# Kernel optimization log

Hardware: AMD Instinct MI355X
Metric: run time of the kernel (lower is better)

## Reference

```python
import jax, jax.numpy as jnp
import numpy as np

V, BLK, L, H, E = 50257, 1024, 12, 12, 768
HS = E // H
B = 2


def _ln(x, w, b, eps=1e-5):
    mu = jnp.mean(x, axis=-1, keepdims=True)
    var = jnp.mean((x - mu) ** 2, axis=-1, keepdims=True)
    return (x - mu) * jax.lax.rsqrt(var + eps) * w + b


def setup_inputs() -> dict:
    key = jax.random.key(0)
    ks = jax.random.split(key, 16)
    s = 0.02
    inp = {
        "x": jax.random.randint(ks[0], (B, BLK), 0, V),
        "tok_emb": jax.random.normal(ks[1], (V, E), jnp.float32) * s,
        "pos_emb": jax.random.normal(ks[2], (BLK, E), jnp.float32) * s,
        "qW": jax.random.normal(ks[3], (L, H, HS, E), jnp.float32) * s,
        "kW": jax.random.normal(ks[4], (L, H, HS, E), jnp.float32) * s,
        "vW": jax.random.normal(ks[5], (L, H, HS, E), jnp.float32) * s,
        "ln1_w": jnp.ones((L, E), jnp.float32),
        "ln1_b": jnp.zeros((L, E), jnp.float32),
        "fc1_w": jax.random.normal(ks[6], (L, 4 * E, E), jnp.float32) * s,
        "fc1_b": jnp.zeros((L, 4 * E), jnp.float32),
        "fc2_w": jax.random.normal(ks[7], (L, E, 4 * E), jnp.float32) * s,
        "fc2_b": jnp.zeros((L, E), jnp.float32),
        "ln2_w": jnp.ones((L, E), jnp.float32),
        "ln2_b": jnp.zeros((L, E), jnp.float32),
        "lnf_w": jnp.ones((E,), jnp.float32),
        "lnf_b": jnp.zeros((E,), jnp.float32),
        "lm_w": jax.random.normal(ks[8], (V, E), jnp.float32) * s,
    }
    return inp


def _gpt(x, tok_emb, pos_emb, qW, kW, vW, ln1_w, ln1_b, fc1_w, fc1_b,
         fc2_w, fc2_b, ln2_w, ln2_b, lnf_w, lnf_b, lm_w):
    T = x.shape[1]
    h = tok_emb[x] + pos_emb[None, :T]  # [B,T,E]
    scale = 1.0 / jnp.sqrt(jnp.asarray(E, h.dtype))  # C**0.5 with C=n_embd
    causal = jnp.tril(jnp.ones((T, T), bool))  # mask where tril==0
    for l in range(L):
        q = jnp.einsum("bte,hde->bthd", h, qW[l])
        k = jnp.einsum("bte,hde->bthd", h, kW[l])
        v = jnp.einsum("bte,hde->bthd", h, vW[l])
        # faithful to source: w = k @ q^T / sqrt(n_embd); rows index k, cols index q
        w = jnp.einsum("bshd,bthd->bhst", k, q) * scale
        w = jnp.where(causal[None, None], w, -jnp.inf)
        w = jax.nn.softmax(w, axis=-1)
        a = jnp.einsum("bhst,bthd->bshd", w, v)  # [B,T,H,HS]
        a = a.reshape(a.shape[0], T, E)  # head-major concat
        h = _ln(h + a, ln1_w[l], ln1_b[l])
        m = jax.nn.gelu(jnp.einsum("bte,fe->btf", h, fc1_w[l]) + fc1_b[l],
                        approximate=False)
        m = jnp.einsum("btf,ef->bte", m, fc2_w[l]) + fc2_b[l]
        h = _ln(h + m, ln2_w[l], ln2_b[l])
    h = _ln(h, lnf_w, lnf_b)
    return jnp.einsum("bte,ve->btv", h, lm_w)


def reference(x, tok_emb, pos_emb, qW, kW, vW, ln1_w, ln1_b, fc1_w, fc1_b,
              fc2_w, fc2_b, ln2_w, ln2_b, lnf_w, lnf_b, lm_w):
    return _gpt(x, tok_emb, pos_emb, qW, kW, vW, ln1_w, ln1_b, fc1_w, fc1_b,
                fc2_w, fc2_b, ln2_w, ln2_b, lnf_w, lnf_b, lm_w)
```

## Files before the change

kernel.cpp:

```cpp
#include <hip/hip_runtime.h>
#include <math.h>

typedef unsigned short u16;
typedef __attribute__((ext_vector_type(8))) short short8;
typedef __attribute__((ext_vector_type(8))) u16 ushort8_t;
typedef __attribute__((ext_vector_type(4))) u16 ushort4_t;
typedef __attribute__((ext_vector_type(4))) float f32x4;

#define BB 2
#define TT 1024
#define EE 768
#define HH 12
#define HSZ 64
#define LL 12
#define FF 3072
#define VV 50257
#define VPAD 50304
#define MM 2048
#define NQKV 2304
#define QKW 1536
#define KVB 128
#define BK 64

__device__ __forceinline__ float bf2f(u16 u) {
    union { unsigned int i; float f; } c;
    c.i = ((unsigned int)u) << 16;
    return c.f;
}
__device__ __forceinline__ u16 f2bf(float f) {
    unsigned int u = __float_as_uint(f);
    unsigned int r = (u + 0x7FFFu + ((u >> 16) & 1u)) >> 16;
    return (u16)r;
}

__device__ __forceinline__ void gload_lds16(const void* g, void* l) {
    __builtin_amdgcn_global_load_lds(
        (const __attribute__((address_space(1))) unsigned int*)g,
        (__attribute__((address_space(3))) unsigned int*)l,
        16, 0, 0);
}

template<int N> __device__ __forceinline__ void waitcnt_vm() {
    if      constexpr (N == 0)  asm volatile("s_waitcnt vmcnt(0)" ::: "memory");
    else if constexpr (N == 4)  asm volatile("s_waitcnt vmcnt(4)" ::: "memory");
    else if constexpr (N == 6)  asm volatile("s_waitcnt vmcnt(6)" ::: "memory");
    else if constexpr (N == 8)  asm volatile("s_waitcnt vmcnt(8)" ::: "memory");
    else if constexpr (N == 12) asm volatile("s_waitcnt vmcnt(12)" ::: "memory");
    else static_assert(N == 0, "unsupported vmcnt");
}

__device__ __forceinline__ void xcd_swizzle(int& bx, int& by) {
    int nx = gridDim.x;
    int nwg = nx * gridDim.y;
    int orig = blockIdx.x + blockIdx.y * nx;
    int q = nwg >> 3, r = nwg & 7;
    int xcd = orig & 7, idx = orig >> 3;
    int nf = (xcd < r ? xcd * (q + 1) : r * (q + 1) + (xcd - r) * q) + idx;
    bx = nf % nx;
    by = nf / nx;
}

__global__ __launch_bounds__(256)
void cast_all_kernel(const float* __restrict__ qW, const float* __restrict__ kW,
                     const float* __restrict__ vW, const float* __restrict__ fc1w,
                     const float* __restrict__ fc2w, const float* __restrict__ lmw,
                     u16* __restrict__ wqkv, u16* __restrict__ wfc1,
                     u16* __restrict__ wfc2, u16* __restrict__ wlm)
{
    const int j = blockIdx.y;
    const float* s;
    u16* d;
    long total, per, stride;
    switch (j) {
    case 0: s = qW;   d = wqkv;              total = (long)LL * EE * EE; per = (long)EE * EE; stride = (long)NQKV * EE; break;
    case 1: s = kW;   d = wqkv + EE * EE;     total = (long)LL * EE * EE; per = (long)EE * EE; stride = (long)NQKV * EE; break;
    case 2: s = vW;   d = wqkv + 2 * EE * EE; total = (long)LL * EE * EE; per = (long)EE * EE; stride = (long)NQKV * EE; break;
    case 3: s = fc1w; d = wfc1;              total = (long)LL * FF * EE; per = total; stride = total; break;
    case 4: s = fc2w; d = wfc2;              total = (long)LL * EE * FF; per = total; stride = total; break;
    default: s = lmw; d = wlm;               total = (long)VV * EE;      per = total; stride = total; break;
    }
    long step = (long)gridDim.x * blockDim.x * 4;
    for (long i = ((long)blockIdx.x * blockDim.x + threadIdx.x) * 4; i < total; i += step) {
        long layer = i / per;
        long off = i - layer * per;
        float4 v = *reinterpret_cast<const float4*>(s + i);
        ushort4_t o;
        o[0] = f2bf(v.x); o[1] = f2bf(v.y); o[2] = f2bf(v.z); o[3] = f2bf(v.w);
        *reinterpret_cast<ushort4_t*>(d + layer * stride + off) = o;
    }
}

__global__ void embed_kernel(const int* __restrict__ x, const float* __restrict__ tok,
                             const float* __restrict__ pos, float* __restrict__ h,
                             u16* __restrict__ hb)
{
    int row = blockIdx.x;
    int t = row & (TT - 1);
    int id = x[row];
    const float* tr = tok + (size_t)id * EE;
    const float* pr = pos + (size_t)t * EE;
    for (int i = threadIdx.x; i < EE; i += blockDim.x) {
        float v = tr[i] + pr[i];
        h[(size_t)row * EE + i] = v;
        hb[(size_t)row * EE + i] = f2bf(v);
    }
}

__global__ __launch_bounds__(256)
void add_ln_kernel(const float* __restrict__ hin, const float* __restrict__ add,
                   const float* __restrict__ add2,
                   const float* __restrict__ w, const float* __restrict__ bias,
                   float* __restrict__ hout, u16* __restrict__ hbout)
{
    int lane = threadIdx.x & 63, wv = threadIdx.x >> 6;
    int row = blockIdx.x * 4 + wv;
    const float* hp = hin + (size_t)row * EE;
    float x[12];
    float s = 0.f;
#pragma unroll
    for (int c = 0; c < 3; ++c) {
        float4 hv = *reinterpret_cast<const float4*>(hp + c * 256 + lane * 4);
        if (add) {
            float4 av = *reinterpret_cast<const float4*>(add + (size_t)row * EE + c * 256 + lane * 4);
            hv.x += av.x; hv.y += av.y; hv.z += av.z; hv.w += av.w;
        }
        if (add2) {
            float4 av = *reinterpret_cast<const float4*>(add2 + (size_t)row * EE + c * 256 + lane * 4);
            hv.x += av.x; hv.y += av.y; hv.z += av.z; hv.w += av.w;
        }
        x[c * 4 + 0] = hv.x; x[c * 4 + 1] = hv.y; x[c * 4 + 2] = hv.z; x[c * 4 + 3] = hv.w;
        s += hv.x + hv.y + hv.z + hv.w;
    }
#pragma unroll
    for (int o = 32; o > 0; o >>= 1) s += __shfl_xor(s, o);
    float mu = s * (1.0f / EE);
    float vs = 0.f;
#pragma unroll
    for (int i = 0; i < 12; ++i) { float d = x[i] - mu; vs += d * d; }
#pragma unroll
    for (int o = 32; o > 0; o >>= 1) vs += __shfl_xor(vs, o);
    float inv = 1.0f / sqrtf(vs * (1.0f / EE) + 1e-5f);
#pragma unroll
    for (int c = 0; c < 3; ++c) {
        int col = c * 256 + lane * 4;
        float4 wv4 = *reinterpret_cast<const float4*>(w + col);
        float4 bv4 = *reinterpret_cast<const float4*>(bias + col);
        float4 o;
        o.x = (x[c * 4 + 0] - mu) * inv * wv4.x + bv4.x;
        o.y = (x[c * 4 + 1] - mu) * inv * wv4.y + bv4.y;
        o.z = (x[c * 4 + 2] - mu) * inv * wv4.z + bv4.z;
        o.w = (x[c * 4 + 3] - mu) * inv * wv4.w + bv4.w;
        *reinterpret_cast<float4*>(hout + (size_t)row * EE + col) = o;
        ushort4_t ob;
        ob[0] = f2bf(o.x); ob[1] = f2bf(o.y); ob[2] = f2bf(o.z); ob[3] = f2bf(o.w);
        *reinterpret_cast<ushort4_t*>(hbout + (size_t)row * EE + col) = ob;
    }
}

enum { EPI_GELU_BF16 = 1, EPI_BIAS_F32 = 2, EPI_F32 = 3, EPI_QKV = 4 };

template<int EPI, bool NGUARD, int DEPTH, int WM, int WN, int MR, int NR, bool KSPLIT = false>
__global__ __launch_bounds__(WM * WN * 64, 2)
void gemm_kernel(const u16* __restrict__ A, const u16* __restrict__ Bw,
                 const float* __restrict__ bias, void* __restrict__ Cout,
                 void* __restrict__ vTout, int Ndim, int Kdim, int Kstride)
{
    constexpr int NW  = WM * WN;
    constexpr int BMT = WM * MR * 16;
    constexpr int BNT = WN * NR * 16;
    constexpr int CA  = BMT / (8 * NW);
    constexpr int CB  = BNT / (8 * NW);
    constexpr int NLD = CA + CB;
    static_assert(BMT % (8 * NW) == 0 && BNT % (8 * NW) == 0, "stage geom");
    __shared__ u16 As[DEPTH * BMT * BK];
    __shared__ u16 Bs[DEPTH * BNT * BK];
    const int tid = threadIdx.x;
    const int lane = tid & 63;
    const int wid = tid >> 6;
    const int wm = wid / WN, wn = wid % WN;
    int bx, by;
    xcd_swizzle(bx, by);
    const int rowBase = bx * BMT;
    const int colBase = by * BNT;

    const u16* Ab = A + (KSPLIT ? (size_t)blockIdx.z * Kdim : 0);
    const u16* Bb = Bw + (KSPLIT ? (size_t)blockIdx.z * Kdim : 0);

    const int srow = lane >> 3;
    const int scol = ((lane & 7) ^ srow) * 8;

#define GSTAGE(k0_, buf_)                                                          \
    {                                                                              \
        _Pragma("unroll")                                                          \
        for (int i_ = 0; i_ < CA; ++i_) {                                          \
            int r0_ = (wid * CA + i_) * 8;                                         \
            gload_lds16(Ab + (size_t)(rowBase + r0_ + srow) * Kstride + (k0_) + scol, \
                        As + (buf_) * (BMT * BK) + r0_ * BK);                      \
        }                                                                          \
        _Pragma("unroll")                                                          \
        for (int i_ = 0; i_ < CB; ++i_) {                                          \
            int r0_ = (wid * CB + i_) * 8;                                         \
            gload_lds16(Bb + (size_t)(colBase + r0_ + srow) * Kstride + (k0_) + scol, \
                        Bs + (buf_) * (BNT * BK) + r0_ * BK);                      \
        }                                                                          \
    }

#define COMPUTE(Asb_, Bsb_)                                                       \
    {                                                                             \
        const int fr = lane & 15;                                                 \
        const int qd = lane >> 4;                                                 \
        _Pragma("unroll")                                                         \
        for (int kk = 0; kk < 2; ++kk) {                                          \
            short8 af[MR], bfr[NR];                                               \
            int goff = (((kk * 4 + qd) ^ (fr & 7))) * 8;                          \
            _Pragma("unroll")                                                     \
            for (int mi = 0; mi < MR; ++mi)                                       \
                af[mi] = *reinterpret_cast<const short8*>(                        \
                    &(Asb_)[(wm * (MR * 16) + mi * 16 + fr) * BK + goff]);        \
            _Pragma("unroll")                                                     \
            for (int ni = 0; ni < NR; ++ni)                                       \
                bfr[ni] = *reinterpret_cast<const short8*>(                       \
                    &(Bsb_)[(wn * (NR * 16) + ni * 16 + fr) * BK + goff]);        \
            _Pragma("unroll")                                                     \
            for (int mi = 0; mi < MR; ++mi)                                       \
                _Pragma("unroll")                                                 \
                for (int ni = 0; ni < NR; ++ni)                                   \
                    acc[mi][ni] = __builtin_amdgcn_mfma_f32_16x16x32_bf16(        \
                        af[mi], bfr[ni], acc[mi][ni], 0, 0, 0);                   \
        }                                                                         \
    }

    f32x4 acc[MR][NR] = {};
    const int nk = Kdim / BK;

    if (DEPTH > 1) {
#pragma unroll
        for (int p = 0; p < DEPTH; ++p) GSTAGE(p * BK, p)
        int cur = 0;
        for (int t = 0; t < nk; ++t) {
            int rem = nk - 1 - t;
            if (rem >= DEPTH - 1)            waitcnt_vm<NLD * (DEPTH - 1)>();
            else if (DEPTH > 2 && rem == 1)  waitcnt_vm<NLD>();
            else                             waitcnt_vm<0>();
            __builtin_amdgcn_s_barrier();
            const u16* Asb = As + cur * (BMT * BK);
            const u16* Bsb = Bs + cur * (BNT * BK);
            COMPUTE(Asb, Bsb)
            __builtin_amdgcn_s_barrier();
            if (t + DEPTH < nk) GSTAGE((t + DEPTH) * BK, cur)
            cur = (cur + 1 == DEPTH) ? 0 : cur + 1;
        }
    } else {
        for (int t = 0; t < nk; ++t) {
            GSTAGE(t * BK, 0)
            __syncthreads();
            COMPUTE(As, Bs)
            __syncthreads();
        }
    }

    if (EPI == EPI_QKV && colBase >= QKW) {
        u16* T = Bs;
        __syncthreads();
#pragma unroll
        for (int mi = 0; mi < MR; ++mi)
#pragma unroll
            for (int ni = 0; ni < NR; ++ni)
#pragma unroll
                for (int r = 0; r < 4; ++r) {
                    int lr = wm * (MR * 16) + mi * 16 + (lane >> 4) * 4 + r;
                    int lc = wn * (NR * 16) + ni * 16 + (lane & 15);
                    T[lc * 72 + lr] = f2bf(acc[mi][ni][r]);
                }
        __syncthreads();
        constexpr int SEGS = BMT / 32;
        int hdl = tid / SEGS;
        int seg = (tid % SEGS) * 32;
        if (hdl < BNT) {
            int b_ = rowBase >> 10;
            int t0 = rowBase & (TT - 1);
            u16* dst = (u16*)vTout + ((size_t)b_ * EE + (colBase - QKW) + hdl) * TT + t0 + seg;
            const u16* src = T + hdl * 72 + seg;
#pragma unroll
            for (int j = 0; j < 4; ++j)
                *reinterpret_cast<ushort8_t*>(dst + j * 8) =
                    *reinterpret_cast<const ushort8_t*>(src + j * 8);
        }
        return;
    }

    const size_t zoff = KSPLIT ? (size_t)blockIdx.z * MM * Ndim : 0;
#pragma unroll
    for (int mi = 0; mi < MR; ++mi) {
#pragma unroll
        for (int ni = 0; ni < NR; ++ni) {
#pragma unroll
            for (int r = 0; r < 4; ++r) {
                int row = rowBase + wm * (MR * 16) + mi * 16 + (lane >> 4) * 4 + r;
                int col = colBase + wn * (NR * 16) + ni * 16 + (lane & 15);
                if (NGUARD && col >= Ndim) continue;
                float v = acc[mi][ni][r];
                if (EPI == EPI_GELU_BF16) { v += bias[col]; v = 0.5f * v * (1.0f + erff(v * 0.70710678f)); }
                if (EPI == EPI_BIAS_F32)  { if (!KSPLIT || blockIdx.z == 0) v += bias[col]; }
                size_t idx = (size_t)row * Ndim + col;
                if (EPI == EPI_QKV) {
                    ((u16*)Cout)[(size_t)row * QKW + col] = f2bf(v);
                } else if (EPI == EPI_GELU_BF16) {
                    ((u16*)Cout)[idx] = f2bf(v);
                } else {
                    ((float*)Cout)[zoff + idx] = v;
                }
            }
        }
    }
}

__global__ __launch_bounds__(256)
void attn_kernel(const u16* __restrict__ qkb, const u16* __restrict__ vT,
                 float* __restrict__ aout)
{
    __shared__ u16 Qs[2 * KVB * 64];
    __shared__ u16 Vs[2 * 64 * KVB];
    __shared__ u16 Ps[4 * 16 * KVB];

    const int lane = threadIdx.x & 63;
    const int wv = threadIdx.x >> 6;
    int bxs, bys;
    xcd_swizzle(bxs, bys);
    const int js = (gridDim.x - 1) - bxs;
    const int s0 = js * 64;
    const int smax = s0 + 63;
    const int bh = bys;
    const int b = bh / HH, h = bh % HH;
    const int bT = b * TT;
    const float scale = 0.036084392f;

    short8 af[2];
    {
        int srow = bT + s0 + wv * 16 + (lane & 15);
#pragma unroll
        for (int kk = 0; kk < 2; ++kk)
            af[kk] = *reinterpret_cast<const short8*>(
                qkb + (size_t)srow * QKW + EE + h * HSZ + kk * 32 + (lane >> 4) * 8);
    }

    const int ntiles = (s0 + 63) / KVB + 1;
    const int qrow = lane >> 3;
    const int qu = lane & 7;
    const int vrow = lane >> 4;
    const int vu = lane & 15;

#define ASTAGE(jt2_, buf_)                                                            \
    {                                                                                 \
        int tb_ = (jt2_) * KVB;                                                       \
        _Pragma("unroll")                                                             \
        for (int i_ = 0; i_ < 4; ++i_) {                                              \
            int R0_ = wv * 32 + i_ * 8;                                               \
            int row_ = R0_ + qrow;                                                    \
            gload_lds16(qkb + (size_t)(bT + tb_ + row_) * QKW + h * HSZ               \
                            + ((qu ^ (row_ & 7)) * 8),                                \
                        &Qs[(buf_) * (KVB * 64) + R0_ * 64]);                         \
        }                                                                             \
        _Pragma("unroll")                                                             \
        for (int i_ = 0; i_ < 4; ++i_) {                                              \
            int R0_ = wv * 16 + i_ * 4;                                               \
            int row_ = R0_ + vrow;                                                    \
            gload_lds16(vT + ((size_t)b * EE + h * HSZ + row_) * TT + tb_             \
                            + ((vu ^ (row_ & 15)) * 8),                               \
                        &Vs[(buf_) * (64 * KVB) + R0_ * KVB]);                        \
        }                                                                             \
    }

    ASTAGE(0, 0)

    float m[4], l[4];
    f32x4 oacc[4] = {};
#pragma unroll
    for (int r = 0; r < 4; ++r) { m[r] = -INFINITY; l[r] = 0.f; }

    int cur = 0;
    for (int jt2 = 0; jt2 < ntiles; ++jt2) {
        __syncthreads();
        if (jt2 + 1 < ntiles) ASTAGE(jt2 + 1, cur ^ 1)

        const u16* Qb = &Qs[cur * (KVB * 64)];
        const u16* Vb = &Vs[cur * (64 * KVB)];
        const int tb = jt2 * KVB;
        const int navail = smax - tb;
        const int nact = min(8, (navail >> 4) + 1);
        const int nkc  = min(4, (navail >> 5) + 1);
        const bool dg = (tb + KVB - 1 > s0);

        f32x4 sc[8];
#pragma unroll
        for (int ni = 0; ni < 8; ++ni) {
            if (ni < nact) {
                f32x4 a = {};
                int trow = ni * 16 + (lane & 15);
#pragma unroll
                for (int kk = 0; kk < 2; ++kk) {
                    int g = kk * 4 + (lane >> 4);
                    short8 bq = *reinterpret_cast<const short8*>(
                        &Qb[trow * 64 + ((g ^ (trow & 7)) * 8)]);
                    a = __builtin_amdgcn_mfma_f32_16x16x32_bf16(af[kk], bq, a, 0, 0, 0);
                }
                sc[ni] = a;
            } else {
                f32x4 mn = {-1e30f, -1e30f, -1e30f, -1e30f};
                sc[ni] = mn;
            }
        }

        if (dg) {
#pragma unroll
            for (int ni = 0; ni < 8; ++ni)
#pragma unroll
                for (int r = 0; r < 4; ++r) {
                    float sv = sc[ni][r] * scale;
                    int t = tb + ni * 16 + (lane & 15);
                    int s = s0 + wv * 16 + (lane >> 4) * 4 + r;
                    if (t > s) sv = -1e30f;
                    sc[ni][r] = sv;
                }
        } else {
#pragma unroll
            for (int ni = 0; ni < 8; ++ni)
#pragma unroll
                for (int r = 0; r < 4; ++r) sc[ni][r] *= scale;
        }

        f32x4 pexp[8];
#pragma unroll
        for (int r = 0; r < 4; ++r) {
            float rm = sc[0][r];
#pragma unroll
            for (int ni = 1; ni < 8; ++ni) rm = fmaxf(rm, sc[ni][r]);
#pragma unroll
            for (int o = 1; o < 16; o <<= 1) rm = fmaxf(rm, __shfl_xor(rm, o));
            float mnew = fmaxf(m[r], rm);
            float alpha = __expf(m[r] - mnew);
            m[r] = mnew;
            float rs = 0.f;
#pragma unroll
            for (int ni = 0; ni < 8; ++ni) {
                float p;
                if (ni < nact) p = __expf(sc[ni][r] - mnew);
                else p = 0.f;
                pexp[ni][r] = p;
                rs += p;
            }
#pragma unroll
            for (int o = 1; o < 16; o <<= 1) rs += __shfl_xor(rs, o);
            l[r] = l[r] * alpha + rs;
#pragma unroll
            for (int dt = 0; dt < 4; ++dt) oacc[dt][r] *= alpha;
        }

        const int nst = nkc * 2;
#pragma unroll
        for (int ni = 0; ni < 8; ++ni) {
            if (ni < nst) {
#pragma unroll
                for (int r = 0; r < 4; ++r) {
                    int sl = (lane >> 4) * 4 + r;
                    int tl = ni * 16 + (lane & 15);
                    Ps[wv * (16 * KVB) + sl * KVB + (((tl >> 3) ^ sl) & 15) * 8 + (tl & 7)]
                        = f2bf(pexp[ni][r]);
                }
            }
        }

#pragma unroll
        for (int kc = 0; kc < 4; ++kc) {
            if (kc < nkc) {
                int srow = lane & 15;
                int g = kc * 4 + (lane >> 4);
                short8 pa = *reinterpret_cast<const short8*>(
                    &Ps[wv * (16 * KVB) + srow * KVB + ((g ^ srow) & 15) * 8]);
#pragma unroll
                for (int dt = 0; dt < 4; ++dt) {
                    int drow = dt * 16 + (lane & 15);
                    short8 bv = *reinterpret_cast<const short8*>(
                        &Vb[drow * KVB + (((kc * 4 + (lane >> 4)) ^ drow) & 15) * 8]);
                    oacc[dt] = __builtin_amdgcn_mfma_f32_16x16x32_bf16(pa, bv, oacc[dt], 0, 0, 0);
                }
            }
        }
        cur ^= 1;
    }

    float invl[4];
#pragma unroll
    for (int r = 0; r < 4; ++r) invl[r] = 1.0f / l[r];
#pragma unroll
    for (int dt = 0; dt < 4; ++dt)
#pragma unroll
        for (int r = 0; r < 4; ++r) {
            int sg = s0 + wv * 16 + (lane >> 4) * 4 + r;
            aout[(size_t)(bT + sg) * EE + h * HSZ + dt * 16 + (lane & 15)] =
                oacc[dt][r] * invl[r];
        }
}

extern "C" void kernel_launch(void* const* d_in, const int* in_sizes, int n_in,
                              void* d_out, int out_size, void* d_ws, size_t ws_size,
                              hipStream_t stream)
{
    const int*   x    = (const int*)d_in[0];
    const float* tok  = (const float*)d_in[1];
    const float* pos  = (const float*)d_in[2];
    const float* qW   = (const float*)d_in[3];
    const float* kW   = (const float*)d_in[4];
    const float* vW   = (const float*)d_in[5];
    const float* ln1w = (const float*)d_in[6];
    const float* ln1b = (const float*)d_in[7];
    const float* fc1w = (const float*)d_in[8];
    const float* fc1b = (const float*)d_in[9];
    const float* fc2w = (const float*)d_in[10];
    const float* fc2b = (const float*)d_in[11];
    const float* ln2w = (const float*)d_in[12];
    const float* ln2b = (const float*)d_in[13];
    const float* lnfw = (const float*)d_in[14];
    const float* lnfb = (const float*)d_in[15];
    const float* lmw  = (const float*)d_in[16];
    float* out = (float*)d_out;

    char* ws = (char*)d_ws;
    u16* wqkv = (u16*)ws;  ws += (size_t)LL * NQKV * EE * 2;
    u16* wfc1 = (u16*)ws;  ws += (size_t)LL * FF * EE * 2;
    u16* wfc2 = (u16*)ws;  ws += (size_t)LL * EE * FF * 2;
    u16* wlm  = (u16*)ws;  ws += (size_t)VPAD * EE * 2;
    float* h    = (float*)ws; ws += (size_t)MM * EE * 4;
    float* tmp  = (float*)ws; ws += (size_t)2 * MM * EE * 4;
    float* tmp2 = tmp + (size_t)MM * EE;
    u16* qkb = (u16*)ws;      ws += (size_t)MM * QKW * 2;
    u16* vTb = (u16*)ws;      ws += (size_t)BB * EE * TT * 2;
    u16* hb  = (u16*)ws;      ws += (size_t)MM * EE * 2;
    u16* mb  = (u16*)ws;      ws += (size_t)MM * FF * 2;

    dim3 blk(256);

    cast_all_kernel<<<dim3(1024, 6), blk, 0, stream>>>(
        qW, kW, vW, fc1w, fc2w, lmw, wqkv, wfc1, wfc2, wlm);

    embed_kernel<<<MM, blk, 0, stream>>>(x, tok, pos, h, hb);

    dim3 gQKV(MM / 64, NQKV / 128);
    dim3 gF1(MM / 64, FF / 128);
    dim3 gF2(MM / 64, EE / 64, 2);
    dim3 gV(MM / 128, VPAD / 128);
    dim3 gAttn(TT / 64, BB * HH);

    for (int l = 0; l < LL; ++l) {
        gemm_kernel<EPI_QKV, false, 2, 2, 2, 2, 4><<<gQKV, blk, 0, stream>>>(
            hb, wqkv + (size_t)l * NQKV * EE, nullptr, qkb, vTb, NQKV, EE, EE);
        attn_kernel<<<gAttn, blk, 0, stream>>>(qkb, vTb, tmp);
        add_ln_kernel<<<MM / 4, blk, 0, stream>>>(h, tmp, nullptr,
                                                  ln1w + l * EE, ln1b + l * EE, h, hb);
        gemm_kernel<EPI_GELU_BF16, false, 2, 2, 2, 2, 4><<<gF1, blk, 0, stream>>>(
            hb, wfc1 + (size_t)l * FF * EE, fc1b + (size_t)l * FF, mb, nullptr, FF, EE, EE);
        gemm_kernel<EPI_BIAS_F32, false, 3, 2, 2, 2, 2, true><<<gF2, blk, 0, stream>>>(
            mb, wfc2 + (size_t)l * EE * FF, fc2b + (size_t)l * EE, tmp, nullptr,
            EE, FF / 2, FF);
        add_ln_kernel<<<MM / 4, blk, 0, stream>>>(h, tmp, tmp2,
                                                  ln2w + l * EE, ln2b + l * EE, h, hb);
    }
    add_ln_kernel<<<MM / 4, blk, 0, stream>>>(h, nullptr, nullptr, lnfw, lnfb, h, hb);
    gemm_kernel<EPI_F32, true, 1, 2, 2, 4, 4><<<gV, blk, 0, stream>>>(
        hb, wlm, nullptr, out, nullptr, VV, EE, EE);
}
```

Before: 1.733 ms.

## Use single-barrier multi-stage pipeline and larger 3-stage tile for LM head GEMM

Rewrites the DEPTH>=3 GEMM main loop so the next stage is issued right after a single barrier, into the buffer consumed in the previous iteration. This removes the second barrier per K-step and keeps DEPTH-1 loads in flight. The DEPTH==2 path is kept as a separate branch. The LM-head GEMM now uses 3-stage buffering with a 4x2 warp grid, 512 threads and 256-row tiles, which halves the grid rows and raises reuse of the large vocab weight. The trade-off is more LDS and registers per block, which may lower occupancy.

```diff
diff --git a/kernel.cpp b/kernel.cpp
--- a/kernel.cpp
+++ b/kernel.cpp
@@ -233,22 +233,31 @@
     f32x4 acc[MR][NR] = {};
     const int nk = Kdim / BK;
 
-    if (DEPTH > 1) {
-#pragma unroll
-        for (int p = 0; p < DEPTH; ++p) GSTAGE(p * BK, p)
-        int cur = 0;
+    if (DEPTH >= 3) {
+#pragma unroll
+        for (int p = 0; p < DEPTH - 1; ++p) GSTAGE(p * BK, p)
         for (int t = 0; t < nk; ++t) {
-            int rem = nk - 1 - t;
-            if (rem >= DEPTH - 1)            waitcnt_vm<NLD * (DEPTH - 1)>();
-            else if (DEPTH > 2 && rem == 1)  waitcnt_vm<NLD>();
-            else                             waitcnt_vm<0>();
+            if (t + 1 < nk) waitcnt_vm<NLD>();
+            else            waitcnt_vm<0>();
             __builtin_amdgcn_s_barrier();
-            const u16* Asb = As + cur * (BMT * BK);
-            const u16* Bsb = Bs + cur * (BNT * BK);
+            if (t + DEPTH - 1 < nk) GSTAGE((t + DEPTH - 1) * BK, (t + DEPTH - 1) % DEPTH)
+            const u16* Asb = As + (t % DEPTH) * (BMT * BK);
+            const u16* Bsb = Bs + (t % DEPTH) * (BNT * BK);
+            COMPUTE(Asb, Bsb)
+        }
+        __syncthreads();
+    } else if (DEPTH == 2) {
+        GSTAGE(0, 0)
+        GSTAGE(BK, 1)
+        for (int t = 0; t < nk; ++t) {
+            if (t + 1 < nk) waitcnt_vm<NLD>();
+            else            waitcnt_vm<0>();
+            __builtin_amdgcn_s_barrier();
+            const u16* Asb = As + (t & 1) * (BMT * BK);
+            const u16* Bsb = Bs + (t & 1) * (BNT * BK);
             COMPUTE(Asb, Bsb)
             __builtin_amdgcn_s_barrier();
-            if (t + DEPTH < nk) GSTAGE((t + DEPTH) * BK, cur)
-            cur = (cur + 1 == DEPTH) ? 0 : cur + 1;
+            if (t + 2 < nk) GSTAGE((t + 2) * BK, t & 1)
         }
     } else {
         for (int t = 0; t < nk; ++t) {
@@ -548,7 +557,7 @@
     dim3 gQKV(MM / 64, NQKV / 128);
     dim3 gF1(MM / 64, FF / 128);
     dim3 gF2(MM / 64, EE / 64, 2);
-    dim3 gV(MM / 128, VPAD / 128);
+    dim3 gV(MM / 256, VPAD / 128);
     dim3 gAttn(TT / 64, BB * HH);
 
     for (int l = 0; l < LL; ++l) {
@@ -566,6 +575,6 @@
                                                   ln2w + l * EE, ln2b + l * EE, h, hb);
     }
     add_ln_kernel<<<MM / 4, blk, 0, stream>>>(h, nullptr, nullptr, lnfw, lnfb, h, hb);
-    gemm_kernel<EPI_F32, true, 1, 2, 2, 4, 4><<<gV, blk, 0, stream>>>(
+    gemm_kernel<EPI_F32, true, 3, 4, 2, 4, 4><<<gV, dim3(512), 0, stream>>>(
         hb, wlm, nullptr, out, nullptr, VV, EE, EE);
 }
```

After: 1.880 ms. 1.09x slower.
